# Kernel optimization log

Hardware: AMD Instinct MI355X
Metric: run time of the kernel (lower is better)

Reference implementation:

```python
import jax, jax.numpy as jnp
import numpy as np

N = 100_000   # nodes
E = 1_600_000 # edges
G, H1, H2, Z = 64, 64, 64, 32


def _w(k, o, i):
    return jax.random.normal(k, (o, i), jnp.float32) * (1.0 / np.sqrt(i))


def setup_inputs() -> dict:
    key = jax.random.key(0)
    ks = jax.random.split(key, 16)
    inp = {
        "x": jax.random.normal(ks[0], (N, G), jnp.float32),
        "edge_src": jax.random.randint(ks[1], (E,), 0, N, jnp.int32),
        "edge_dst": jax.random.randint(ks[2], (E,), 0, N, jnp.int32),
        "eps": jax.random.normal(ks[3], (N, Z), jnp.float32),
        "W1": _w(ks[4], H1, G),  "b1": jnp.zeros((H1,), jnp.float32),
        "W2": _w(ks[5], H2, H1), "b2": jnp.zeros((H2,), jnp.float32),
        "W31": _w(ks[6], Z, H2), "b31": jnp.zeros((Z,), jnp.float32),
        "W32": _w(ks[7], Z, H2), "b32": jnp.zeros((Z,), jnp.float32),
        "W4": _w(ks[8], H2, Z),  "b4": jnp.zeros((H2,), jnp.float32),
        "W5": _w(ks[9], H1, H2), "b5": jnp.zeros((H1,), jnp.float32),
        "W6": _w(ks[10], G, H1), "b6": jnp.zeros((G,), jnp.float32),
    }
    return inp


def _gcn(h, W, b, act, src, dst, norm):
    # message: h_src * norm_src, gathered per edge  [E, d]
    m = (h * norm)[src]
    # reduce: sum over incoming edges, scaled by norm_dst  [N, d]
    agg = jax.ops.segment_sum(m, dst, num_segments=N) * norm
    # node apply: linear + activation
    return act(agg @ W.T + b)


def reference(x, edge_src, edge_dst, eps,
              W1, b1, W2, b2, W31, b31, W32, b32, W4, b4, W5, b5, W6, b6):
    # symmetric GCN norm: deg^{-1/2} from in-degree
    deg = jax.ops.segment_sum(jnp.ones((E,), jnp.float32), edge_dst, num_segments=N)
    norm = jax.lax.rsqrt(jnp.maximum(deg, 1.0))[:, None]  # [N,1]

    relu = jax.nn.relu
    ident = lambda h: h

    h = _gcn(x, W1, b1, relu, edge_src, edge_dst, norm)
    h = _gcn(h, W2, b2, relu, edge_src, edge_dst, norm)
    mu = _gcn(h, W31, b31, ident, edge_src, edge_dst, norm)
    log_var = _gcn(h, W32, b32, ident, edge_src, edge_dst, norm)

    z = eps * jnp.exp(0.5 * log_var) + mu

    h = _gcn(z, W4, b4, relu, edge_src, edge_dst, norm)
    h = _gcn(h, W5, b5, relu, edge_src, edge_dst, norm)
    recon = _gcn(h, W6, b6, jax.nn.sigmoid, edge_src, edge_dst, norm)
    return recon, mu, log_var
```

## Files before the change

kernel.cpp:

```cpp
#include <hip/hip_runtime.h>
#include <hip/hip_fp16.h>
#include <math.h>

#define NN 100000
#define NE 1600000
#define NBKT 391
#define CHUNK 8192
#define NB1 ((NE + CHUNK - 1) / CHUNK)
#define HALFN 50000

typedef _Float16 v8h __attribute__((ext_vector_type(8)));
typedef float v4f __attribute__((ext_vector_type(4)));

__global__ __launch_bounds__(256) void p0_hist_kernel(const int* __restrict__ dst,
                                                      int* __restrict__ bcnt) {
    __shared__ int h[NBKT];
    for (int b = threadIdx.x; b < NBKT; b += 256) h[b] = 0;
    __syncthreads();
    int e0 = blockIdx.x * CHUNK;
    for (int k = 0; k < CHUNK / 256; ++k) {
        int e = e0 + threadIdx.x + k * 256;
        if (e < NE) atomicAdd(&h[dst[e] >> 8], 1);
    }
    __syncthreads();
    for (int b = threadIdx.x; b < NBKT; b += 256)
        if (h[b]) atomicAdd(&bcnt[b], h[b]);
}

__global__ void scan_buckets_kernel(const int* __restrict__ bcnt, int* __restrict__ bbase,
                                    int* __restrict__ bcur) {
    __shared__ int s[512];
    int tid = threadIdx.x;
    int v = (tid < NBKT) ? bcnt[tid] : 0;
    s[tid] = v;
    __syncthreads();
    for (int off = 1; off < 512; off <<= 1) {
        int t = (tid >= off) ? s[tid - off] : 0;
        __syncthreads();
        s[tid] += t;
        __syncthreads();
    }
    if (tid < NBKT) { int ex = s[tid] - v; bbase[tid] = ex; bcur[tid] = ex; }
    if (tid == NBKT) bbase[NBKT] = NE;
}

__global__ __launch_bounds__(256) void p1_scatter_kernel(const int* __restrict__ src,
                                                         const int* __restrict__ dst,
                                                         int* __restrict__ bcur,
                                                         int* __restrict__ gpair) {
    __shared__ int h[NBKT], rb[NBKT], hc[NBKT];
    int tid = threadIdx.x;
    for (int b = tid; b < NBKT; b += 256) { h[b] = 0; hc[b] = 0; }
    __syncthreads();
    int e0 = blockIdx.x * CHUNK;
    for (int k = 0; k < CHUNK / 256; ++k) {
        int e = e0 + tid + k * 256;
        if (e < NE) atomicAdd(&h[dst[e] >> 8], 1);
    }
    __syncthreads();
    for (int b = tid; b < NBKT; b += 256)
        rb[b] = h[b] ? atomicAdd(&bcur[b], h[b]) : 0;
    __syncthreads();
    for (int k = 0; k < CHUNK / 256; ++k) {
        int e = e0 + tid + k * 256;
        if (e < NE) {
            int d = dst[e], s = src[e];
            int b = d >> 8;
            int pos = rb[b] + atomicAdd(&hc[b], 1);
            gpair[pos] = (s << 8) | (d & 255);
        }
    }
}

__global__ __launch_bounds__(256) void p2_place_kernel(const int* __restrict__ gpair,
                                                       const int* __restrict__ bbase,
                                                       int* __restrict__ csr,
                                                       int* __restrict__ row_start,
                                                       int* __restrict__ row_mid,
                                                       float* __restrict__ nrm) {
    __shared__ int cnt[256], cntLo[256], nexcl[256], baseL[256], baseH[256], pl[256], ph[256];
    int b = blockIdx.x, tid = threadIdx.x;
    int s0 = bbase[b], s1 = bbase[b + 1];
    cnt[tid] = 0; cntLo[tid] = 0; pl[tid] = 0; ph[tid] = 0;
    __syncthreads();
    for (int i = s0 + tid; i < s1; i += 256) {
        int p = gpair[i];
        int l = p & 255;
        atomicAdd(&cnt[l], 1);
        if ((p >> 8) < HALFN) atomicAdd(&cntLo[l], 1);
    }
    __syncthreads();
    int v = cnt[tid];
    nexcl[tid] = v;
    __syncthreads();
    for (int off = 1; off < 256; off <<= 1) {
        int t = (tid >= off) ? nexcl[tid - off] : 0;
        __syncthreads();
        nexcl[tid] += t;
        __syncthreads();
    }
    int ex = nexcl[tid] - v;
    int base = s0 + ex;
    int node = (b << 8) + tid;
    if (node < NN) {
        row_start[node] = base;
        row_mid[node]   = base + cntLo[tid];
        nrm[node] = rsqrtf(fmaxf((float)v, 1.0f));
    }
    if (b == NBKT - 1 && tid == 0) row_start[NN] = NE;
    baseL[tid] = base;
    baseH[tid] = base + cntLo[tid];
    __syncthreads();
    for (int i = s0 + tid; i < s1; i += 256) {
        int p = gpair[i];
        int l = p & 255;
        int s = p >> 8;
        int pos = (s < HALFN) ? (baseL[l] + atomicAdd(&pl[l], 1))
                              : (baseH[l] + atomicAdd(&ph[l], 1));
        csr[pos] = s;
    }
}

union H4 { uint2 u; __half2 h[2]; };

__global__ void scale_x_h_kernel(const float4* __restrict__ x4, const float* __restrict__ nrm,
                                 uint2* __restrict__ xs, int total4) {
    int i = blockIdx.x * blockDim.x + threadIdx.x;
    if (i < total4) {
        float nv = nrm[i >> 4];
        float4 v = x4[i];
        H4 w;
        w.h[0] = __floats2half2_rn(v.x * nv, v.y * nv);
        w.h[1] = __floats2half2_rn(v.z * nv, v.w * nv);
        xs[i] = w.u;
    }
}

template<int IN, bool ACC>
__global__ __launch_bounds__(256) void gcn_gather_kernel(
        const __half* __restrict__ h,
        const int* __restrict__ rs_arr, const int* __restrict__ re_arr,
        const int* __restrict__ csr,
        uint2* __restrict__ pAgg) {
    constexpr int MLP = 8;
    constexpr int RL  = IN / 4;
    constexpr int EPI = 64 / RL;
    int tid = threadIdx.x;
    int wave = tid >> 6, lane = tid & 63;
    int row_slot = lane / RL;
    int f4 = lane % RL;
    int nodeBase = (blockIdx.x * 4 + wave) * MLP;
    const uint2* hp = (const uint2*)h;

    int rsb[MLP], re[MLP];
#pragma unroll
    for (int i = 0; i < MLP; ++i) {
        rsb[i] = rs_arr[nodeBase + i];
        re[i]  = re_arr[nodeBase + i];
    }
    int maxd = 0;
#pragma unroll
    for (int i = 0; i < MLP; ++i) maxd = max(maxd, re[i] - rsb[i]);
#pragma unroll
    for (int i = 0; i < MLP; ++i) rsb[i] += row_slot;

    float4 acc[MLP];
#pragma unroll
    for (int i = 0; i < MLP; ++i) acc[i] = make_float4(0.f, 0.f, 0.f, 0.f);

    for (int t = 0; t < maxd; t += EPI) {
        int s[MLP]; float m[MLP];
#pragma unroll
        for (int i = 0; i < MLP; ++i) {
            int jj = rsb[i] + t;
            bool ok = jj < re[i];
            s[i] = csr[ok ? jj : 0];
            m[i] = ok ? 1.f : 0.f;
        }
        H4 v[MLP];
#pragma unroll
        for (int i = 0; i < MLP; ++i)
            v[i].u = hp[(size_t)s[i] * RL + f4];
#pragma unroll
        for (int i = 0; i < MLP; ++i) {
            float2 f01 = __half22float2(v[i].h[0]);
            float2 f23 = __half22float2(v[i].h[1]);
            acc[i].x = fmaf(m[i], f01.x, acc[i].x);
            acc[i].y = fmaf(m[i], f01.y, acc[i].y);
            acc[i].z = fmaf(m[i], f23.x, acc[i].z);
            acc[i].w = fmaf(m[i], f23.y, acc[i].w);
        }
    }

#pragma unroll
    for (int i = 0; i < MLP; ++i) {
        for (int o = RL; o < 64; o <<= 1) {
            acc[i].x += __shfl_xor(acc[i].x, o);
            acc[i].y += __shfl_xor(acc[i].y, o);
            acc[i].z += __shfl_xor(acc[i].z, o);
            acc[i].w += __shfl_xor(acc[i].w, o);
        }
    }

    if (row_slot == 0) {
        if (ACC) {
            uint2 old[MLP];
#pragma unroll
            for (int i = 0; i < MLP; ++i)
                old[i] = pAgg[(size_t)(nodeBase + i) * RL + f4];
#pragma unroll
            for (int i = 0; i < MLP; ++i) {
                H4 o4; o4.u = old[i];
                float2 a01 = __half22float2(o4.h[0]);
                float2 a23 = __half22float2(o4.h[1]);
                acc[i].x += a01.x; acc[i].y += a01.y;
                acc[i].z += a23.x; acc[i].w += a23.y;
            }
        }
#pragma unroll
        for (int i = 0; i < MLP; ++i) {
            H4 w;
            w.h[0] = __floats2half2_rn(acc[i].x, acc[i].y);
            w.h[1] = __floats2half2_rn(acc[i].z, acc[i].w);
            pAgg[(size_t)(nodeBase + i) * RL + f4] = w.u;
        }
    }
}

template<int IN, int ACT, bool SCALE, bool DUAL>
__global__ __launch_bounds__(256) void gcn_apply_mfma_kernel(
        const __half* __restrict__ pAgg,
        const float* __restrict__ nrm,
        const float* __restrict__ Wa, const float* __restrict__ ba,
        const float* __restrict__ Wb, const float* __restrict__ bb,
        void* __restrict__ outv, float* __restrict__ out2,
        const float* __restrict__ eps, __half* __restrict__ zbuf) {
    constexpr int KH = IN / 32;
    int tid = threadIdx.x;
    int wave = tid >> 6, lane = tid & 63;
    int col = lane & 15, kgrp = lane >> 4;

    v8h Bhi[4][KH], Blo[4][KH];
    float bias[4];
#pragma unroll
    for (int t = 0; t < 4; ++t) {
        const float* wrow;
        if (DUAL) wrow = (t < 2) ? (Wa + (size_t)(t * 16 + col) * 64)
                                 : (Wb + (size_t)((t - 2) * 16 + col) * 64);
        else      wrow = Wa + (size_t)(t * 16 + col) * IN;
        bias[t] = DUAL ? ((t < 2) ? ba[t * 16 + col] : bb[(t - 2) * 16 + col])
                       : ba[t * 16 + col];
#pragma unroll
        for (int kh = 0; kh < KH; ++kh) {
            const float* wp = wrow + kh * 32 + kgrp * 8;
            float4 w0 = *(const float4*)(wp);
            float4 w1 = *(const float4*)(wp + 4);
            float wv[8] = {w0.x, w0.y, w0.z, w0.w, w1.x, w1.y, w1.z, w1.w};
#pragma unroll
            for (int j = 0; j < 8; ++j) {
                _Float16 hv = (_Float16)wv[j];
                Bhi[t][kh][j] = hv;
                Blo[t][kh][j] = (_Float16)(wv[j] - (float)hv);
            }
        }
    }

    int base = blockIdx.x * 128 + wave * 32;
    const _Float16* ag = (const _Float16*)pAgg;
    v4f acc[2][4];
#pragma unroll
    for (int a2 = 0; a2 < 2; ++a2)
#pragma unroll
        for (int t = 0; t < 4; ++t)
            acc[a2][t] = (v4f){0.f, 0.f, 0.f, 0.f};

#pragma unroll
    for (int a2 = 0; a2 < 2; ++a2) {
        int arow = base + a2 * 16 + col;
        if (arow > NN - 1) arow = NN - 1;
        const _Float16* arp = ag + (size_t)arow * IN + kgrp * 8;
        v8h A0 = *(const v8h*)(arp);
        v8h A1{};
        if constexpr (KH == 2) A1 = *(const v8h*)(arp + 32);
#pragma unroll
        for (int t = 0; t < 4; ++t) {
            acc[a2][t] = __builtin_amdgcn_mfma_f32_16x16x32_f16(A0, Bhi[t][0], acc[a2][t], 0, 0, 0);
            acc[a2][t] = __builtin_amdgcn_mfma_f32_16x16x32_f16(A0, Blo[t][0], acc[a2][t], 0, 0, 0);
            if constexpr (KH == 2) {
                acc[a2][t] = __builtin_amdgcn_mfma_f32_16x16x32_f16(A1, Bhi[t][1], acc[a2][t], 0, 0, 0);
                acc[a2][t] = __builtin_amdgcn_mfma_f32_16x16x32_f16(A1, Blo[t][1], acc[a2][t], 0, 0, 0);
            }
        }
    }

#pragma unroll
    for (int a2 = 0; a2 < 2; ++a2) {
#pragma unroll
        for (int r = 0; r < 4; ++r) {
            int node = base + a2 * 16 + kgrp * 4 + r;
            if (node >= NN) continue;
            float nv = nrm[node];
            float oa[4];
#pragma unroll
            for (int t = 0; t < 4; ++t) {
                float v = acc[a2][t][r] * nv + bias[t];
                if (ACT == 1) v = fmaxf(v, 0.f);
                if (ACT == 2) v = 1.f / (1.f + expf(-v));
                oa[t] = v;
            }
            if (DUAL) {
                float* mu_p = (float*)outv;
#pragma unroll
                for (int t = 0; t < 2; ++t) {
                    int zo = t * 16 + col;
                    float muv = oa[t], lvv = oa[t + 2];
                    mu_p[(size_t)node * 32 + zo] = muv;
                    out2[(size_t)node * 32 + zo] = lvv;
                    float e = eps[(size_t)node * 32 + zo];
                    zbuf[(size_t)node * 32 + zo] = __float2half((e * expf(0.5f * lvv) + muv) * nv);
                }
            } else if (SCALE) {
                __half* op = (__half*)outv + (size_t)node * 64 + col;
#pragma unroll
                for (int t = 0; t < 4; ++t) op[t * 16] = __float2half(oa[t] * nv);
            } else {
                float* op = (float*)outv + (size_t)node * 64 + col;
#pragma unroll
                for (int t = 0; t < 4; ++t) op[t * 16] = oa[t];
            }
        }
    }
}

extern "C" void kernel_launch(void* const* d_in, const int* in_sizes, int n_in,
                              void* d_out, int out_size, void* d_ws, size_t ws_size,
                              hipStream_t stream) {
    const float* x    = (const float*)d_in[0];
    const int*   esrc = (const int*)d_in[1];
    const int*   edst = (const int*)d_in[2];
    const float* eps  = (const float*)d_in[3];
    const float* W1  = (const float*)d_in[4];  const float* b1  = (const float*)d_in[5];
    const float* W2  = (const float*)d_in[6];  const float* b2  = (const float*)d_in[7];
    const float* W31 = (const float*)d_in[8];  const float* b31 = (const float*)d_in[9];
    const float* W32 = (const float*)d_in[10]; const float* b32 = (const float*)d_in[11];
    const float* W4  = (const float*)d_in[12]; const float* b4  = (const float*)d_in[13];
    const float* W5  = (const float*)d_in[14]; const float* b5  = (const float*)d_in[15];
    const float* W6  = (const float*)d_in[16]; const float* b6  = (const float*)d_in[17];

    float* outp  = (float*)d_out;
    float* recon = outp;
    float* mu    = outp + (size_t)NN * 64;
    float* lv    = mu   + (size_t)NN * 32;

    int* wsI       = (int*)d_ws;
    int* bcnt      = wsI;
    int* bbase     = bcnt + 392;
    int* bcur      = bbase + 392;
    int* row_start = bcur + 392;
    int* row_mid   = row_start + NN + 4;
    int* csr       = row_mid + NN + 4;
    float* nrm     = (float*)(csr + NE);
    __half* pAgg   = (__half*)(nrm + NN);
    __half* hA     = pAgg + (size_t)NN * 64;
    __half* hB     = hA + (size_t)NN * 64;
    int* gpair     = (int*)pAgg;

    const int SB = 256;
    const int fgrid = NN / 32;
    const int agrid = (NN + 127) / 128;

    hipMemsetAsync(bcnt, 0, 392 * sizeof(int), stream);
    p0_hist_kernel<<<NB1, 256, 0, stream>>>(edst, bcnt);
    scan_buckets_kernel<<<1, 512, 0, stream>>>(bcnt, bbase, bcur);
    p1_scatter_kernel<<<NB1, 256, 0, stream>>>(esrc, edst, bcur, gpair);
    p2_place_kernel<<<NBKT, 256, 0, stream>>>(gpair, bbase, csr, row_start, row_mid, nrm);

    scale_x_h_kernel<<<(NN * 16 + SB - 1) / SB, SB, 0, stream>>>((const float4*)x, nrm, (uint2*)hA, NN * 16);

    uint2* pW = (uint2*)pAgg;
    const __half* pH = (const __half*)pAgg;
    const int* rm = row_mid;
    const int* rsA = row_start;
    const int* reA = row_start + 1;

    gcn_gather_kernel<64, false><<<fgrid, 256, 0, stream>>>(hA, rsA, rm, csr, pW);
    gcn_gather_kernel<64, true ><<<fgrid, 256, 0, stream>>>(hA, rm, reA, csr, pW);
    gcn_apply_mfma_kernel<64, 1, true,  false><<<agrid, 256, 0, stream>>>(pH, nrm, W1,  b1,  nullptr, nullptr, hB,    nullptr, nullptr, nullptr);
    gcn_gather_kernel<64, false><<<fgrid, 256, 0, stream>>>(hB, rsA, rm, csr, pW);
    gcn_gather_kernel<64, true ><<<fgrid, 256, 0, stream>>>(hB, rm, reA, csr, pW);
    gcn_apply_mfma_kernel<64, 1, true,  false><<<agrid, 256, 0, stream>>>(pH, nrm, W2,  b2,  nullptr, nullptr, hA,    nullptr, nullptr, nullptr);
    gcn_gather_kernel<64, false><<<fgrid, 256, 0, stream>>>(hA, rsA, rm, csr, pW);
    gcn_gather_kernel<64, true ><<<fgrid, 256, 0, stream>>>(hA, rm, reA, csr, pW);
    gcn_apply_mfma_kernel<64, 0, false, true ><<<agrid, 256, 0, stream>>>(pH, nrm, W31, b31, W32,     b32,     mu,    lv,      eps,     hB);
    gcn_gather_kernel<32, false><<<fgrid, 256, 0, stream>>>(hB, rsA, rm, csr, pW);
    gcn_gather_kernel<32, true ><<<fgrid, 256, 0, stream>>>(hB, rm, reA, csr, pW);
    gcn_apply_mfma_kernel<32, 1, true,  false><<<agrid, 256, 0, stream>>>(pH, nrm, W4,  b4,  nullptr, nullptr, hA,    nullptr, nullptr, nullptr);
    gcn_gather_kernel<64, false><<<fgrid, 256, 0, stream>>>(hA, rsA, rm, csr, pW);
    gcn_gather_kernel<64, true ><<<fgrid, 256, 0, stream>>>(hA, rm, reA, csr, pW);
    gcn_apply_mfma_kernel<64, 1, true,  false><<<agrid, 256, 0, stream>>>(pH, nrm, W5,  b5,  nullptr, nullptr, hB,    nullptr, nullptr, nullptr);
    gcn_gather_kernel<64, false><<<fgrid, 256, 0, stream>>>(hB, rsA, rm, csr, pW);
    gcn_gather_kernel<64, true ><<<fgrid, 256, 0, stream>>>(hB, rm, reA, csr, pW);
    gcn_apply_mfma_kernel<64, 2, false, false><<<agrid, 256, 0, stream>>>(pH, nrm, W6,  b6,  nullptr, nullptr, recon, nullptr, nullptr, nullptr);
}
```

Measured before the change: 577.4 us.

## Merge split gather passes into one kernel iterating four source-range segments

The CSR rows are now split into four sub-ranges by source-node quarter instead of two halves, and a single gather kernel walks all four segments in sequence. Previously two gather launches per layer handled the low and high halves, the second reading back and adding the half-precision partial result. The aim is cache locality on the source feature table, with each segment touching a quarter of it, while dropping the extra launch and the partial-sum round trip. The cost is more per-segment loop overhead and more padded iterations from per-segment max-degree divergence across the eight nodes.

```diff
diff --git a/kernel.cpp b/kernel.cpp
--- a/kernel.cpp
+++ b/kernel.cpp
@@ -7,7 +7,8 @@
 #define NBKT 391
 #define CHUNK 8192
 #define NB1 ((NE + CHUNK - 1) / CHUNK)
-#define HALFN 50000
+#define QSEG 25000
+#define NNP (NN + 8)
 
 typedef _Float16 v8h __attribute__((ext_vector_type(8)));
 typedef float v4f __attribute__((ext_vector_type(4)));
@@ -75,22 +76,22 @@
 __global__ __launch_bounds__(256) void p2_place_kernel(const int* __restrict__ gpair,
                                                        const int* __restrict__ bbase,
                                                        int* __restrict__ csr,
-                                                       int* __restrict__ row_start,
-                                                       int* __restrict__ row_mid,
+                                                       int* __restrict__ seg,
                                                        float* __restrict__ nrm) {
-    __shared__ int cnt[256], cntLo[256], nexcl[256], baseL[256], baseH[256], pl[256], ph[256];
+    __shared__ int cseg[4][256], nexcl[256], sb[4][256], pq[4][256];
     int b = blockIdx.x, tid = threadIdx.x;
     int s0 = bbase[b], s1 = bbase[b + 1];
-    cnt[tid] = 0; cntLo[tid] = 0; pl[tid] = 0; ph[tid] = 0;
+#pragma unroll
+    for (int q = 0; q < 4; ++q) { cseg[q][tid] = 0; pq[q][tid] = 0; }
     __syncthreads();
     for (int i = s0 + tid; i < s1; i += 256) {
         int p = gpair[i];
         int l = p & 255;
-        atomicAdd(&cnt[l], 1);
-        if ((p >> 8) < HALFN) atomicAdd(&cntLo[l], 1);
-    }
-    __syncthreads();
-    int v = cnt[tid];
+        int q = (p >> 8) / QSEG;
+        atomicAdd(&cseg[q][l], 1);
+    }
+    __syncthreads();
+    int v = cseg[0][tid] + cseg[1][tid] + cseg[2][tid] + cseg[3][tid];
     nexcl[tid] = v;
     __syncthreads();
     for (int off = 1; off < 256; off <<= 1) {
@@ -102,21 +103,26 @@
     int ex = nexcl[tid] - v;
     int base = s0 + ex;
     int node = (b << 8) + tid;
+    int c0 = cseg[0][tid], c1 = cseg[1][tid], c2 = cseg[2][tid];
     if (node < NN) {
-        row_start[node] = base;
-        row_mid[node]   = base + cntLo[tid];
+        seg[0 * NNP + node] = base;
+        seg[1 * NNP + node] = base + c0;
+        seg[2 * NNP + node] = base + c0 + c1;
+        seg[3 * NNP + node] = base + c0 + c1 + c2;
+        seg[4 * NNP + node] = base + v;
         nrm[node] = rsqrtf(fmaxf((float)v, 1.0f));
     }
-    if (b == NBKT - 1 && tid == 0) row_start[NN] = NE;
-    baseL[tid] = base;
-    baseH[tid] = base + cntLo[tid];
+    sb[0][tid] = base;
+    sb[1][tid] = base + c0;
+    sb[2][tid] = base + c0 + c1;
+    sb[3][tid] = base + c0 + c1 + c2;
     __syncthreads();
     for (int i = s0 + tid; i < s1; i += 256) {
         int p = gpair[i];
         int l = p & 255;
         int s = p >> 8;
-        int pos = (s < HALFN) ? (baseL[l] + atomicAdd(&pl[l], 1))
-                              : (baseH[l] + atomicAdd(&ph[l], 1));
+        int q = s / QSEG;
+        int pos = sb[q][l] + atomicAdd(&pq[q][l], 1);
         csr[pos] = s;
     }
 }
@@ -136,10 +142,10 @@
     }
 }
 
-template<int IN, bool ACC>
-__global__ __launch_bounds__(256) void gcn_gather_kernel(
+template<int IN>
+__global__ __launch_bounds__(256) void gcn_gather4_kernel(
         const __half* __restrict__ h,
-        const int* __restrict__ rs_arr, const int* __restrict__ re_arr,
+        const int* __restrict__ seg,
         const int* __restrict__ csr,
         uint2* __restrict__ pAgg) {
     constexpr int MLP = 8;
@@ -152,44 +158,47 @@
     int nodeBase = (blockIdx.x * 4 + wave) * MLP;
     const uint2* hp = (const uint2*)h;
 
-    int rsb[MLP], re[MLP];
-#pragma unroll
-    for (int i = 0; i < MLP; ++i) {
-        rsb[i] = rs_arr[nodeBase + i];
-        re[i]  = re_arr[nodeBase + i];
-    }
-    int maxd = 0;
-#pragma unroll
-    for (int i = 0; i < MLP; ++i) maxd = max(maxd, re[i] - rsb[i]);
-#pragma unroll
-    for (int i = 0; i < MLP; ++i) rsb[i] += row_slot;
-
     float4 acc[MLP];
 #pragma unroll
     for (int i = 0; i < MLP; ++i) acc[i] = make_float4(0.f, 0.f, 0.f, 0.f);
 
-    for (int t = 0; t < maxd; t += EPI) {
-        int s[MLP]; float m[MLP];
-#pragma unroll
-        for (int i = 0; i < MLP; ++i) {
-            int jj = rsb[i] + t;
-            bool ok = jj < re[i];
-            s[i] = csr[ok ? jj : 0];
-            m[i] = ok ? 1.f : 0.f;
-        }
-        H4 v[MLP];
-#pragma unroll
-        for (int i = 0; i < MLP; ++i)
-            v[i].u = hp[(size_t)s[i] * RL + f4];
-#pragma unroll
-        for (int i = 0; i < MLP; ++i) {
-            float2 f01 = __half22float2(v[i].h[0]);
-            float2 f23 = __half22float2(v[i].h[1]);
-            acc[i].x = fmaf(m[i], f01.x, acc[i].x);
-            acc[i].y = fmaf(m[i], f01.y, acc[i].y);
-            acc[i].z = fmaf(m[i], f23.x, acc[i].z);
-            acc[i].w = fmaf(m[i], f23.y, acc[i].w);
-        }
+    int cur[MLP];
+#pragma unroll
+    for (int i = 0; i < MLP; ++i) cur[i] = seg[nodeBase + i];
+
+    for (int q = 0; q < 4; ++q) {
+        int nxt[MLP];
+#pragma unroll
+        for (int i = 0; i < MLP; ++i) nxt[i] = seg[(q + 1) * NNP + nodeBase + i];
+        int maxd = 0;
+#pragma unroll
+        for (int i = 0; i < MLP; ++i) maxd = max(maxd, nxt[i] - cur[i]);
+
+        for (int t = 0; t < maxd; t += EPI) {
+            int s[MLP]; float m[MLP];
+#pragma unroll
+            for (int i = 0; i < MLP; ++i) {
+                int jj = cur[i] + t + row_slot;
+                bool ok = jj < nxt[i];
+                s[i] = csr[ok ? jj : 0];
+                m[i] = ok ? 1.f : 0.f;
+            }
+            H4 v[MLP];
+#pragma unroll
+            for (int i = 0; i < MLP; ++i)
+                v[i].u = hp[(size_t)s[i] * RL + f4];
+#pragma unroll
+            for (int i = 0; i < MLP; ++i) {
+                float2 f01 = __half22float2(v[i].h[0]);
+                float2 f23 = __half22float2(v[i].h[1]);
+                acc[i].x = fmaf(m[i], f01.x, acc[i].x);
+                acc[i].y = fmaf(m[i], f01.y, acc[i].y);
+                acc[i].z = fmaf(m[i], f23.x, acc[i].z);
+                acc[i].w = fmaf(m[i], f23.y, acc[i].w);
+            }
+        }
+#pragma unroll
+        for (int i = 0; i < MLP; ++i) cur[i] = nxt[i];
     }
 
 #pragma unroll
@@ -203,20 +212,6 @@
     }
 
     if (row_slot == 0) {
-        if (ACC) {
-            uint2 old[MLP];
-#pragma unroll
-            for (int i = 0; i < MLP; ++i)
-                old[i] = pAgg[(size_t)(nodeBase + i) * RL + f4];
-#pragma unroll
-            for (int i = 0; i < MLP; ++i) {
-                H4 o4; o4.u = old[i];
-                float2 a01 = __half22float2(o4.h[0]);
-                float2 a23 = __half22float2(o4.h[1]);
-                acc[i].x += a01.x; acc[i].y += a01.y;
-                acc[i].z += a23.x; acc[i].w += a23.y;
-            }
-        }
 #pragma unroll
         for (int i = 0; i < MLP; ++i) {
             H4 w;
@@ -356,9 +351,8 @@
     int* bcnt      = wsI;
     int* bbase     = bcnt + 392;
     int* bcur      = bbase + 392;
-    int* row_start = bcur + 392;
-    int* row_mid   = row_start + NN + 4;
-    int* csr       = row_mid + NN + 4;
+    int* seg       = bcur + 392;
+    int* csr       = seg + 5 * NNP;
     float* nrm     = (float*)(csr + NE);
     __half* pAgg   = (__half*)(nrm + NN);
     __half* hA     = pAgg + (size_t)NN * 64;
@@ -373,32 +367,23 @@
     p0_hist_kernel<<<NB1, 256, 0, stream>>>(edst, bcnt);
     scan_buckets_kernel<<<1, 512, 0, stream>>>(bcnt, bbase, bcur);
     p1_scatter_kernel<<<NB1, 256, 0, stream>>>(esrc, edst, bcur, gpair);
-    p2_place_kernel<<<NBKT, 256, 0, stream>>>(gpair, bbase, csr, row_start, row_mid, nrm);
+    p2_place_kernel<<<NBKT, 256, 0, stream>>>(gpair, bbase, csr, seg, nrm);
 
     scale_x_h_kernel<<<(NN * 16 + SB - 1) / SB, SB, 0, stream>>>((const float4*)x, nrm, (uint2*)hA, NN * 16);
 
     uint2* pW = (uint2*)pAgg;
     const __half* pH = (const __half*)pAgg;
-    const int* rm = row_mid;
-    const int* rsA = row_start;
-    const int* reA = row_start + 1;
-
-    gcn_gather_kernel<64, false><<<fgrid, 256, 0, stream>>>(hA, rsA, rm, csr, pW);
-    gcn_gather_kernel<64, true ><<<fgrid, 256, 0, stream>>>(hA, rm, reA, csr, pW);
+
+    gcn_gather4_kernel<64><<<fgrid, 256, 0, stream>>>(hA, seg, csr, pW);
     gcn_apply_mfma_kernel<64, 1, true,  false><<<agrid, 256, 0, stream>>>(pH, nrm, W1,  b1,  nullptr, nullptr, hB,    nullptr, nullptr, nullptr);
-    gcn_gather_kernel<64, false><<<fgrid, 256, 0, stream>>>(hB, rsA, rm, csr, pW);
-    gcn_gather_kernel<64, true ><<<fgrid, 256, 0, stream>>>(hB, rm, reA, csr, pW);
+    gcn_gather4_kernel<64><<<fgrid, 256, 0, stream>>>(hB, seg, csr, pW);
     gcn_apply_mfma_kernel<64, 1, true,  false><<<agrid, 256, 0, stream>>>(pH, nrm, W2,  b2,  nullptr, nullptr, hA,    nullptr, nullptr, nullptr);
-    gcn_gather_kernel<64, false><<<fgrid, 256, 0, stream>>>(hA, rsA, rm, csr, pW);
-    gcn_gather_kernel<64, true ><<<fgrid, 256, 0, stream>>>(hA, rm, reA, csr, pW);
+    gcn_gather4_kernel<64><<<fgrid, 256, 0, stream>>>(hA, seg, csr, pW);
     gcn_apply_mfma_kernel<64, 0, false, true ><<<agrid, 256, 0, stream>>>(pH, nrm, W31, b31, W32,     b32,     mu,    lv,      eps,     hB);
-    gcn_gather_kernel<32, false><<<fgrid, 256, 0, stream>>>(hB, rsA, rm, csr, pW);
-    gcn_gather_kernel<32, true ><<<fgrid, 256, 0, stream>>>(hB, rm, reA, csr, pW);
+    gcn_gather4_kernel<32><<<fgrid, 256, 0, stream>>>(hB, seg, csr, pW);
     gcn_apply_mfma_kernel<32, 1, true,  false><<<agrid, 256, 0, stream>>>(pH, nrm, W4,  b4,  nullptr, nullptr, hA,    nullptr, nullptr, nullptr);
-    gcn_gather_kernel<64, false><<<fgrid, 256, 0, stream>>>(hA, rsA, rm, csr, pW);
-    gcn_gather_kernel<64, true ><<<fgrid, 256, 0, stream>>>(hA, rm, reA, csr, pW);
+    gcn_gather4_kernel<64><<<fgrid, 256, 0, stream>>>(hA, seg, csr, pW);
     gcn_apply_mfma_kernel<64, 1, true,  false><<<agrid, 256, 0, stream>>>(pH, nrm, W5,  b5,  nullptr, nullptr, hB,    nullptr, nullptr, nullptr);
-    gcn_gather_kernel<64, false><<<fgrid, 256, 0, stream>>>(hB, rsA, rm, csr, pW);
-    gcn_gather_kernel<64, true ><<<fgrid, 256, 0, stream>>>(hB, rm, reA, csr, pW);
+    gcn_gather4_kernel<64><<<fgrid, 256, 0, stream>>>(hB, seg, csr, pW);
     gcn_apply_mfma_kernel<64, 2, false, false><<<agrid, 256, 0, stream>>>(pH, nrm, W6,  b6,  nullptr, nullptr, recon, nullptr, nullptr, nullptr);
 }
```

Measured after the change: 553.1 us. 4.2% less time.
